# Kernel tuning notes

Measured on AMD Instinct MI355X. Metric: run time of the kernel, lower is better.

Reference implementation:

```python
import jax, jax.numpy as jnp
import numpy as np

BATCH = 8
NDATA = 8192
NPOINT = 1024
NSAMPLE = 32
RADIUS = 0.2
CFEAT = 64


def setup_inputs() -> dict:
    key = jax.random.key(0)
    k1, k2, k3 = jax.random.split(key, 3)
    new_xyz = jax.random.normal(k1, (BATCH, NPOINT, 3), dtype=jnp.float32)
    xyz = jax.random.normal(k2, (BATCH, NDATA, 3), dtype=jnp.float32)
    points = jax.random.normal(k3, (BATCH, NDATA, CFEAT), dtype=jnp.float32)
    return {"new_xyz": new_xyz, "xyz": xyz, "points": points}


def reference(new_xyz, xyz, points):
    # Pairwise distances from every centroid to every dataset point.
    # delta: [B, P, N, 3]
    delta = xyz[:, None, :, :] - new_xyz[:, :, None, :]
    dist = jnp.linalg.norm(delta, axis=-1)  # [B, P, N]

    # Sort by distance (the original does a full argsort per centroid).
    sorted_idx = jnp.argsort(dist, axis=-1).astype(jnp.int32)  # [B, P, N]
    sorted_d = jnp.take_along_axis(dist, sorted_idx, axis=-1)  # [B, P, N]

    # Nearest point index replaces out-of-radius slots.
    nearest = sorted_idx[:, :, 0:1]  # [B, P, 1]
    radius_idx = jnp.where(sorted_d < RADIUS, sorted_idx, nearest)
    idx = radius_idx[:, :, :NSAMPLE]  # [B, P, S] int32 (ndataset >= nsample)

    # Batched gathers: grouped_xyz [B, P, S, 3], grouped_points [B, P, S, C].
    grouped_xyz = jnp.take_along_axis(
        xyz[:, None, :, :], idx[..., None], axis=2)
    grouped_points = jnp.take_along_axis(
        points[:, None, :, :], idx[..., None], axis=2)
    new_points = jnp.concatenate([grouped_xyz, grouped_points], axis=-1)
    return (new_points, idx, grouped_xyz)
```

## Files before the change

kernel.cpp:

```cpp
#include <hip/hip_runtime.h>
#include <math.h>

typedef unsigned int   u32;
typedef unsigned long long u64;

#define BATCH   8
#define NDATA   8192
#define NPOINT  1024
#define NSAMPLE 32
#define CFEAT   64
#define ROWF    67
#define MAXCAND 128
#define QPW     2
#define QPB     8
#define TILE    512
#define DWT     (TILE*3)
#define NT      (NDATA/TILE)
#define PLANE   516

#define OUT_IDX (BATCH*NPOINT*NSAMPLE*ROWF)
#define OUT_GX  (OUT_IDX + BATCH*NPOINT*NSAMPLE)

__device__ __forceinline__ float rnbf(float f) {
    u32 b = __float_as_uint(f);
    b += 0x7FFFu + ((b >> 16) & 1u);
    return __uint_as_float(b & 0xFFFF0000u);
}
__device__ __forceinline__ int clampidx(int v) {
    return (v < 0) ? 0 : (v > NDATA-1 ? NDATA-1 : v);
}

__global__ __launch_bounds__(256, 4)
void grouping_kernel(const float* __restrict__ new_xyz,
                     const float* __restrict__ xyz,
                     const float* __restrict__ points,
                     float* __restrict__ out, float T)
{
    __shared__ __align__(16) float S[2][3*PLANE];
    __shared__ float cand_s[QPB][MAXCAND];
    __shared__ int   cand_i[QPB][MAXCAND];
    __shared__ int   sel[QPB][NSAMPLE];

    const int tid  = threadIdx.x;
    const int wv   = tid >> 6;
    const int lane = tid & 63;
    const int q0   = blockIdx.x * QPB + wv * QPW;
    const int b    = q0 >> 10;

    sel[wv*QPW + (lane >> 5)][lane & 31] = 0;

    float qx[QPW], qy[QPW], qz[QPW];
    #pragma unroll
    for (int j = 0; j < QPW; ++j) {
        qx[j] = new_xyz[(q0+j)*3 + 0];
        qy[j] = new_xyz[(q0+j)*3 + 1];
        qz[j] = new_xyz[(q0+j)*3 + 2];
    }
    const float* bx = xyz + (size_t)b * NDATA * 3;

    #pragma unroll
    for (int k = 0; k < DWT/256; ++k) {
        int w = k*256 + tid;
        int p = w / 3, c = w - 3*p;
        S[0][c*PLANE + p] = bx[w];
    }
    __syncthreads();

    int n[QPW]; n[0] = 0; n[1] = 0;
    for (int t = 0; t < NT; ++t) {
        const int cur = t & 1, nxt = cur ^ 1;
        if (t + 1 < NT) {
            #pragma unroll
            for (int k = 0; k < DWT/256; ++k) {
                int w = k*256 + tid;
                int p = w / 3, c = w - 3*p;
                S[nxt][c*PLANE + p] = bx[(t+1)*DWT + w];
            }
        }
        #pragma unroll
        for (int u = 0; u < TILE/256; ++u) {
            const float4 xv = ((const float4*)(S[cur]          ))[u*64 + lane];
            const float4 yv = ((const float4*)(S[cur] +   PLANE))[u*64 + lane];
            const float4 zv = ((const float4*)(S[cur] + 2*PLANE))[u*64 + lane];
            float d2v[QPW][4];
            u64   mv [QPW][4];
            u64 ored = 0;
            #pragma unroll
            for (int j = 0; j < 4; ++j) {
                float x = (&xv.x)[j], y = (&yv.x)[j], z = (&zv.x)[j];
                #pragma unroll
                for (int s = 0; s < QPW; ++s) {
                    float dx = __fsub_rn(x, qx[s]);
                    float dy = __fsub_rn(y, qy[s]);
                    float dz = __fsub_rn(z, qz[s]);
                    float d2 = __fadd_rn(__fadd_rn(__fmul_rn(dx,dx), __fmul_rn(dy,dy)),
                                         __fmul_rn(dz,dz));
                    d2v[s][j] = d2;
                    u64 m = __ballot(d2 < T);
                    mv[s][j] = m;
                    ored |= m;
                }
            }
            if (ored) {
                #pragma unroll
                for (int s = 0; s < QPW; ++s) {
                    #pragma unroll
                    for (int j = 0; j < 4; ++j) {
                        u64 m = mv[s][j];
                        if (m) {
                            if (d2v[s][j] < T) {
                                int below = __builtin_amdgcn_mbcnt_hi((u32)(m >> 32),
                                             __builtin_amdgcn_mbcnt_lo((u32)m, 0));
                                int pos = n[s] + below;
                                if (pos < MAXCAND) {
                                    cand_s[wv*QPW + s][pos] = __fsqrt_rn(d2v[s][j]);
                                    cand_i[wv*QPW + s][pos] = t*TILE + u*256 + 4*lane + j;
                                }
                            }
                            n[s] += (int)__popcll(m);
                        }
                    }
                }
            }
        }
        __syncthreads();
    }

    int mini[QPW]; mini[0] = 0; mini[1] = 0;
    #pragma unroll
    for (int s = 0; s < QPW; ++s) {
        if (n[s] == 0) {
            float mind = 3.402823466e38f; int mi = 0;
            for (int k = 0; k < NDATA/64; ++k) {
                int i = (k << 6) + lane;
                float dx = __fsub_rn(bx[i*3+0], qx[s]);
                float dy = __fsub_rn(bx[i*3+1], qy[s]);
                float dz = __fsub_rn(bx[i*3+2], qz[s]);
                float d2 = __fadd_rn(__fadd_rn(__fmul_rn(dx,dx), __fmul_rn(dy,dy)),
                                     __fmul_rn(dz,dz));
                if (d2 < mind) { mind = d2; mi = i; }
            }
            float ms = __fsqrt_rn(mind);
            for (int off = 32; off; off >>= 1) {
                float os = __shfl_xor(ms, off);
                int   oi = __shfl_xor(mi, off);
                if (os < ms || (os == ms && oi < mi)) { ms = os; mi = oi; }
            }
            mini[s] = mi;
        }
    }

    __syncthreads();

    #pragma unroll
    for (int s = 0; s < QPW; ++s) {
        const int wq = wv*QPW + s;
        const int nj = n[s] > MAXCAND ? MAXCAND : n[s];
        for (int kk = lane; kk < nj; kk += 64) {
            float sk = cand_s[wq][kk];
            int   ik = cand_i[wq][kk];
            int r = 0;
            for (int mm = 0; mm < nj; ++mm) {
                float sm = cand_s[wq][mm];
                int   im = cand_i[wq][mm];
                r += (int)((sm < sk) | ((sm == sk) & (im < ik)));
            }
            if (r < NSAMPLE) sel[wq][r] = clampidx(ik);
        }
    }
    __syncthreads();
    #pragma unroll
    for (int s = 0; s < QPW; ++s) {
        const int wq = wv*QPW + s;
        const int nj = n[s] > MAXCAND ? MAXCAND : n[s];
        const int nsel = nj < NSAMPLE ? nj : NSAMPLE;
        if (lane >= nsel && lane < NSAMPLE) {
            int pad = (nj > 0) ? sel[wq][0] : clampidx(mini[s]);
            sel[wq][lane] = pad;
        }
    }
    __syncthreads();

    const float* prow = points + (size_t)b * NDATA * CFEAT;
    #pragma unroll
    for (int s = 0; s < QPW; ++s) {
        const int q  = q0 + s;
        const int wq = wv*QPW + s;

        if (lane < NSAMPLE)
            out[OUT_IDX + (size_t)q*NSAMPLE + lane] = rnbf((float)sel[wq][lane]);

        for (int e = lane; e < NSAMPLE*3; e += 64) {
            int sR = e / 3, c2 = e - sR*3;
            int is = sel[wq][sR];
            out[OUT_GX + (size_t)q*(NSAMPLE*3) + e] = rnbf(bx[is*3 + c2]);
        }

        float* onp = out + (size_t)q * (NSAMPLE*ROWF);
        for (int e = lane; e < NSAMPLE*ROWF; e += 64) {
            int sR = e / ROWF;
            int c2 = e - sR*ROWF;
            int is = sel[wq][sR];
            const float* ap = (c2 < 3) ? (bx + (size_t)is*3 + c2)
                                       : (prow + (size_t)is*CFEAT + (c2-3));
            onp[e] = rnbf(*ap);
        }
    }
}

extern "C" void kernel_launch(void* const* d_in, const int* in_sizes, int n_in,
                              void* d_out, int out_size, void* d_ws, size_t ws_size,
                              hipStream_t stream) {
    union { u32 u; float f; } lo, hi, mid;
    lo.u = 0u; hi.f = 0.05f;
    while (hi.u - lo.u > 1u) {
        mid.u = lo.u + (hi.u - lo.u) / 2u;
        if (sqrtf(mid.f) >= 0.2f) hi.u = mid.u; else lo.u = mid.u;
    }
    float T = hi.f;

    grouping_kernel<<<(BATCH*NPOINT)/QPB, 256, 0, stream>>>(
        (const float*)d_in[0],
        (const float*)d_in[1],
        (const float*)d_in[2],
        (float*)d_out, T);
}
```

Measured before the change: 136.6 us.

## Keep AoS tile layout with float4 copies, halve block size, simplify ballot path

The shared xyz tile is now a straight float4 copy of the interleaved AoS data instead of being transposed into padded SoA planes. Each lane reads three float4s and unpacks its four points' x/y/z in registers. Blocks shrink to 128 threads with 4 queries each, doubling the block count, and the two-pass ballot/OR-reduce candidate logic is folded into a single per-ballot branch. This removes the divide-by-3 scatter and strided LDS writes during staging. In exchange each block now stages the full tile for only 4 queries, so xyz global traffic doubles, and LDS reads at a 48-byte lane stride may hit bank conflicts.

```diff
diff --git a/kernel.cpp b/kernel.cpp
--- a/kernel.cpp
+++ b/kernel.cpp
@@ -12,11 +12,11 @@
 #define ROWF    67
 #define MAXCAND 128
 #define QPW     2
-#define QPB     8
+#define QPB     4
 #define TILE    512
 #define DWT     (TILE*3)
+#define F4T     (DWT/4)
 #define NT      (NDATA/TILE)
-#define PLANE   516
 
 #define OUT_IDX (BATCH*NPOINT*NSAMPLE*ROWF)
 #define OUT_GX  (OUT_IDX + BATCH*NPOINT*NSAMPLE)
@@ -30,13 +30,13 @@
     return (v < 0) ? 0 : (v > NDATA-1 ? NDATA-1 : v);
 }
 
-__global__ __launch_bounds__(256, 4)
+__global__ __launch_bounds__(128, 8)
 void grouping_kernel(const float* __restrict__ new_xyz,
                      const float* __restrict__ xyz,
                      const float* __restrict__ points,
                      float* __restrict__ out, float T)
 {
-    __shared__ __align__(16) float S[2][3*PLANE];
+    __shared__ __align__(16) float S[2][DWT];
     __shared__ float cand_s[QPB][MAXCAND];
     __shared__ int   cand_i[QPB][MAXCAND];
     __shared__ int   sel[QPB][NSAMPLE];
@@ -47,23 +47,21 @@
     const int q0   = blockIdx.x * QPB + wv * QPW;
     const int b    = q0 >> 10;
 
-    sel[wv*QPW + (lane >> 5)][lane & 31] = 0;
+    sel[tid >> 5][tid & 31] = 0;
 
     float qx[QPW], qy[QPW], qz[QPW];
     #pragma unroll
-    for (int j = 0; j < QPW; ++j) {
-        qx[j] = new_xyz[(q0+j)*3 + 0];
-        qy[j] = new_xyz[(q0+j)*3 + 1];
-        qz[j] = new_xyz[(q0+j)*3 + 2];
+    for (int s = 0; s < QPW; ++s) {
+        qx[s] = new_xyz[(q0+s)*3 + 0];
+        qy[s] = new_xyz[(q0+s)*3 + 1];
+        qz[s] = new_xyz[(q0+s)*3 + 2];
     }
     const float* bx = xyz + (size_t)b * NDATA * 3;
-
-    #pragma unroll
-    for (int k = 0; k < DWT/256; ++k) {
-        int w = k*256 + tid;
-        int p = w / 3, c = w - 3*p;
-        S[0][c*PLANE + p] = bx[w];
-    }
+    const float4* src4 = (const float4*)bx;
+
+    #pragma unroll
+    for (int k = 0; k < F4T/128; ++k)
+        ((float4*)S[0])[k*128 + tid] = src4[k*128 + tid];
     __syncthreads();
 
     int n[QPW]; n[0] = 0; n[1] = 0;
@@ -71,54 +69,37 @@
         const int cur = t & 1, nxt = cur ^ 1;
         if (t + 1 < NT) {
             #pragma unroll
-            for (int k = 0; k < DWT/256; ++k) {
-                int w = k*256 + tid;
-                int p = w / 3, c = w - 3*p;
-                S[nxt][c*PLANE + p] = bx[(t+1)*DWT + w];
-            }
+            for (int k = 0; k < F4T/128; ++k)
+                ((float4*)S[nxt])[k*128 + tid] = src4[(t+1)*F4T + k*128 + tid];
         }
         #pragma unroll
         for (int u = 0; u < TILE/256; ++u) {
-            const float4 xv = ((const float4*)(S[cur]          ))[u*64 + lane];
-            const float4 yv = ((const float4*)(S[cur] +   PLANE))[u*64 + lane];
-            const float4 zv = ((const float4*)(S[cur] + 2*PLANE))[u*64 + lane];
-            float d2v[QPW][4];
-            u64   mv [QPW][4];
-            u64 ored = 0;
+            const float4* tq = ((const float4*)S[cur]) + (u*192 + 3*lane);
+            float4 r0 = tq[0], r1 = tq[1], r2 = tq[2];
+            float xs[4] = {r0.x, r0.w, r1.z, r2.y};
+            float ys[4] = {r0.y, r1.x, r1.w, r2.z};
+            float zs[4] = {r0.z, r1.y, r2.x, r2.w};
             #pragma unroll
             for (int j = 0; j < 4; ++j) {
-                float x = (&xv.x)[j], y = (&yv.x)[j], z = (&zv.x)[j];
                 #pragma unroll
                 for (int s = 0; s < QPW; ++s) {
-                    float dx = __fsub_rn(x, qx[s]);
-                    float dy = __fsub_rn(y, qy[s]);
-                    float dz = __fsub_rn(z, qz[s]);
+                    float dx = __fsub_rn(xs[j], qx[s]);
+                    float dy = __fsub_rn(ys[j], qy[s]);
+                    float dz = __fsub_rn(zs[j], qz[s]);
                     float d2 = __fadd_rn(__fadd_rn(__fmul_rn(dx,dx), __fmul_rn(dy,dy)),
                                          __fmul_rn(dz,dz));
-                    d2v[s][j] = d2;
                     u64 m = __ballot(d2 < T);
-                    mv[s][j] = m;
-                    ored |= m;
-                }
-            }
-            if (ored) {
-                #pragma unroll
-                for (int s = 0; s < QPW; ++s) {
-                    #pragma unroll
-                    for (int j = 0; j < 4; ++j) {
-                        u64 m = mv[s][j];
-                        if (m) {
-                            if (d2v[s][j] < T) {
-                                int below = __builtin_amdgcn_mbcnt_hi((u32)(m >> 32),
-                                             __builtin_amdgcn_mbcnt_lo((u32)m, 0));
-                                int pos = n[s] + below;
-                                if (pos < MAXCAND) {
-                                    cand_s[wv*QPW + s][pos] = __fsqrt_rn(d2v[s][j]);
-                                    cand_i[wv*QPW + s][pos] = t*TILE + u*256 + 4*lane + j;
-                                }
+                    if (m) {
+                        if (d2 < T) {
+                            int below = __builtin_amdgcn_mbcnt_hi((u32)(m >> 32),
+                                         __builtin_amdgcn_mbcnt_lo((u32)m, 0));
+                            int pos = n[s] + below;
+                            if (pos < MAXCAND) {
+                                cand_s[wv*QPW + s][pos] = __fsqrt_rn(d2);
+                                cand_i[wv*QPW + s][pos] = t*TILE + u*256 + 4*lane + j;
                             }
-                            n[s] += (int)__popcll(m);
                         }
+                        n[s] += (int)__popcll(m);
                     }
                 }
             }
@@ -219,7 +200,7 @@
     }
     float T = hi.f;
 
-    grouping_kernel<<<(BATCH*NPOINT)/QPB, 256, 0, stream>>>(
+    grouping_kernel<<<(BATCH*NPOINT)/QPB, 128, 0, stream>>>(
         (const float*)d_in[0],
         (const float*)d_in[1],
         (const float*)d_in[2],
```

New measurement: 138.8 us. About the same (+1.6%).
